# Kernel optimization log

Hardware: AMD Instinct MI355X
Metric: run time of the kernel (lower is better)

The kernel has to match this reference:

```python
import jax, jax.numpy as jnp
import numpy as np

T = 1024          # tokens (batch*seq, vLLM flattened layout)
D = 2048          # hidden_size
H = 16            # attention heads
HD = D // H       # head_dim = 128
E = 16            # num routed experts
K = 2             # top_k
IM = 1408         # moe_intermediate_size
IS = 5632         # shared_expert_intermediate_size
EPS = 1e-6
THETA = 10000.0


def setup_inputs() -> dict:
    key = jax.random.key(0)
    ks = jax.random.split(key, 14)
    s = 0.02  # weight scale
    n = jax.random.normal
    return {
        "positions": jnp.arange(T, dtype=jnp.int32),
        "hidden_states": n(ks[0], (T, D), jnp.float32),
        "ln1_w": 1.0 + s * n(ks[1], (D,), jnp.float32),
        "ln2_w": 1.0 + s * n(ks[2], (D,), jnp.float32),
        "qkv_w": s * n(ks[3], (D, 3 * H * HD), jnp.float32),
        "qkv_b": s * n(ks[4], (3 * H * HD,), jnp.float32),
        "o_w": s * n(ks[5], (H * HD, D), jnp.float32),
        "router_w": s * n(ks[6], (D, E), jnp.float32),
        "w_gate": s * n(ks[7], (E, D, IM), jnp.float32),
        "w_up": s * n(ks[8], (E, D, IM), jnp.float32),
        "w_down": s * n(ks[9], (E, IM, D), jnp.float32),
        "sh_gate_up": s * n(ks[10], (D, 2 * IS), jnp.float32),
        "sh_down": s * n(ks[11], (IS, D), jnp.float32),
        "sh_expert_gate": s * n(ks[12], (D, 1), jnp.float32),
    }


def _rmsnorm(x, w):
    var = jnp.mean(x * x, axis=-1, keepdims=True)
    return x * jax.lax.rsqrt(var + EPS) * w


def _rope(x, positions):
    # neox-style rotary: x [T, H, HD]
    half = HD // 2
    inv_freq = 1.0 / (THETA ** (jnp.arange(0, half, dtype=jnp.float32) / half * 1.0))
    inv_freq = 1.0 / (THETA ** (jnp.arange(0, HD, 2, dtype=jnp.float32) / HD))
    ang = positions.astype(jnp.float32)[:, None] * inv_freq  # [T, HD/2]
    cos = jnp.cos(ang)[:, None, :]
    sin = jnp.sin(ang)[:, None, :]
    x1, x2 = x[..., :half], x[..., half:]
    return jnp.concatenate([x1 * cos - x2 * sin, x2 * cos + x1 * sin], axis=-1)


def reference(positions, hidden_states, ln1_w, ln2_w, qkv_w, qkv_b, o_w,
              router_w, w_gate, w_up, w_down, sh_gate_up, sh_down,
              sh_expert_gate):
    # --- input RMSNorm (residual=None path) ---
    residual = hidden_states
    x = _rmsnorm(hidden_states, ln1_w)

    # --- self-attention: QKV + RoPE + causal SDPA + o_proj ---
    qkv = x @ qkv_w + qkv_b
    q, k, v = jnp.split(qkv, [H * HD, 2 * H * HD], axis=-1)
    q = _rope(q.reshape(T, H, HD), positions)
    k = _rope(k.reshape(T, H, HD), positions)
    v = v.reshape(T, H, HD)
    scale = HD ** -0.5
    scores = jnp.einsum('thd,shd->hts', q, k) * scale  # [H, T, T]
    causal = jnp.tril(jnp.ones((T, T), dtype=bool))
    scores = jnp.where(causal[None], scores, jnp.finfo(scores.dtype).min)
    attn = jax.nn.softmax(scores, axis=-1)
    ctx = jnp.einsum('hts,shd->thd', attn, v).reshape(T, H * HD)
    attn_out = ctx @ o_w

    # --- fused add + post-attention RMSNorm ---
    residual = residual + attn_out
    x = _rmsnorm(residual, ln2_w)

    # --- sparse MoE: router -> softmax -> top-k (renormalized) -> experts ---
    logits = x @ router_w                                    # [T, E]
    probs = jax.nn.softmax(logits.astype(jnp.float32), axis=-1)
    topv, topi = jax.lax.top_k(probs, K)                     # [T, K]
    topv = topv / jnp.sum(topv, axis=-1, keepdims=True)      # norm_topk_prob
    w = jnp.zeros((T, E), dtype=x.dtype).at[
        jnp.arange(T)[:, None], topi].set(topv.astype(x.dtype))
    g = jax.nn.silu(jnp.einsum('td,edi->tei', x, w_gate)) * \
        jnp.einsum('td,edi->tei', x, w_up)                   # [T, E, IM]
    moe_out = jnp.einsum('tei,eid,te->td', g, w_down, w)

    # --- shared expert with sigmoid gate ---
    gu = x @ sh_gate_up
    g2, u2 = jnp.split(gu, 2, axis=-1)
    shared = (jax.nn.silu(g2) * u2) @ sh_down
    shared = jax.nn.sigmoid(x @ sh_expert_gate) * shared

    hidden_states = moe_out + shared
    return hidden_states, residual
```

## Files before the change

### kernel.cpp

```cpp
#include <hip/hip_runtime.h>

constexpr int T_  = 1024;
constexpr int D_  = 2048;
constexpr int H_  = 16;
constexpr int HD_ = 128;
constexpr int E_  = 16;
constexpr int IM_ = 1408;
constexpr int IS_ = 5632;

typedef __attribute__((ext_vector_type(8))) short bf16x8;
typedef __attribute__((ext_vector_type(4))) short short4v;
typedef __attribute__((ext_vector_type(4))) float f32x4;

__device__ __forceinline__ short f2bf(float f){
  unsigned u = __builtin_bit_cast(unsigned, f);
  u += 0x7fffu + ((u >> 16) & 1u);
  return (short)(u >> 16);
}
__device__ __forceinline__ float bf2f(short s){
  unsigned u = ((unsigned)(unsigned short)s) << 16;
  return __builtin_bit_cast(float, u);
}
__device__ __forceinline__ f32x4 mfma16(bf16x8 a, bf16x8 b, f32x4 c){
  return __builtin_amdgcn_mfma_f32_16x16x32_bf16(a, b, c, 0, 0, 0);
}
__device__ __forceinline__ void split3(float f, short& h, short& m, short& l){
  h = f2bf(f); float r = f - bf2f(h);
  m = f2bf(r); l = f2bf(r - bf2f(m));
}
__device__ __forceinline__ void split2(float f, short& h, short& m){
  h = f2bf(f); m = f2bf(f - bf2f(h));
}

__global__ __launch_bounds__(256) void sctab_kernel(
    const int* __restrict__ pos, float* __restrict__ cst, float* __restrict__ snt)
{
  int idx = blockIdx.x * 256 + threadIdx.x;
  if (idx >= T_ * 64) return;
  int t = idx >> 6, i = idx & 63;
  float invf = (float)pow(10000.0, -(double)i / 64.0);
  float ang  = (float)pos[t] * invf;
  double s, c;
  sincos((double)ang, &s, &c);
  cst[idx] = (float)c; snt[idx] = (float)s;
}

__global__ __launch_bounds__(256) void rms_kernel(
    const float* __restrict__ x, const float* __restrict__ w,
    short* __restrict__ o0, short* __restrict__ o1, short* __restrict__ o2,
    short* __restrict__ ob, float* __restrict__ of)
{
  int t = blockIdx.x, tid = threadIdx.x;
  const float* xr = x + (size_t)t * D_;
  float4 va = ((const float4*)xr)[tid*2];
  float4 vb = ((const float4*)xr)[tid*2+1];
  float ss = va.x*va.x + va.y*va.y + va.z*va.z + va.w*va.w
           + vb.x*vb.x + vb.y*vb.y + vb.z*vb.z + vb.w*vb.w;
  for (int o = 32; o; o >>= 1) ss += __shfl_xor(ss, o, 64);
  __shared__ float red[4];
  int lane = tid & 63, wid = tid >> 6;
  if (lane == 0) red[wid] = ss;
  __syncthreads();
  ss = red[0] + red[1] + red[2] + red[3];
  float rs = 1.0f / sqrtf(ss * (1.0f/D_) + 1e-6f);
  float4 wa = ((const float4*)w)[tid*2];
  float4 wb = ((const float4*)w)[tid*2+1];
  float xv[8] = {va.x,va.y,va.z,va.w, vb.x,vb.y,vb.z,vb.w};
  float wv[8] = {wa.x,wa.y,wa.z,wa.w, wb.x,wb.y,wb.z,wb.w};
  size_t base = (size_t)t * D_ + tid*8;
  for (int j = 0; j < 8; ++j){
    float o = xv[j] * rs * wv[j];
    if (o0){
      short hh, mm, ll; split3(o, hh, mm, ll);
      o0[base+j] = hh; o1[base+j] = mm; o2[base+j] = ll;
    }
    if (ob) ob[base+j] = f2bf(o);
    if (of) of[base+j] = o;
  }
}

__global__ __launch_bounds__(256) void prepk_kernel(
    const float* __restrict__ qkv, const float* __restrict__ cst,
    const float* __restrict__ snt, short* __restrict__ Kp0, short* __restrict__ Kp1)
{
  int idx = blockIdx.x * 256 + threadIdx.x;
  int c = idx & 7, t = (idx >> 3) & (T_-1), h = idx >> 13;
  int d0 = c * 8;
  const float* kp = qkv + (size_t)t * (3*D_) + D_ + h*HD_;
  const float* cp = cst + t*64 + d0;
  const float* sp = snt + t*64 + d0;
  bf16x8 lh, ll, hh, hl;
  #pragma unroll
  for (int j = 0; j < 8; ++j){
    float xl = kp[d0+j], xh = kp[d0+64+j];
    float cv = cp[j], sv = sp[j];
    float rl = xl*cv - xh*sv, rh = xh*cv + xl*sv;
    short a, b;
    split2(rl, a, b); lh[j] = a; ll[j] = b;
    split2(rh, a, b); hh[j] = a; hl[j] = b;
  }
  size_t ob = ((size_t)h*T_ + t) * HD_;
  *(bf16x8*)(Kp0 + ob + d0)      = lh;
  *(bf16x8*)(Kp0 + ob + 64 + d0) = hh;
  *(bf16x8*)(Kp1 + ob + d0)      = ll;
  *(bf16x8*)(Kp1 + ob + 64 + d0) = hl;
}

__global__ __launch_bounds__(256) void prepv_kernel(
    const float* __restrict__ qkv, short* __restrict__ Vp0, short* __restrict__ Vp1)
{
  __shared__ short Vl[2][128][72];
  int t0 = blockIdx.x * 64, h = blockIdx.y, tid = threadIdx.x;
  int r = tid >> 2, cq = (tid & 3) * 32;
  const float* src = qkv + (size_t)(t0+r) * (3*D_) + 2*D_ + h*HD_ + cq;
  #pragma unroll
  for (int jj = 0; jj < 8; ++jj){
    float4 v = *(const float4*)(src + jj*4);
    float vv[4] = {v.x, v.y, v.z, v.w};
    #pragma unroll
    for (int u = 0; u < 4; ++u){
      int d = cq + jj*4 + u;
      short a, b; split2(vv[u], a, b);
      Vl[0][d][r] = a; Vl[1][d][r] = b;
    }
  }
  __syncthreads();
  int d = tid >> 1, tc = (tid & 1) * 32;
  short* dst0 = Vp0 + ((size_t)h*HD_ + d) * T_ + t0 + tc;
  short* dst1 = Vp1 + ((size_t)h*HD_ + d) * T_ + t0 + tc;
  #pragma unroll
  for (int q = 0; q < 4; ++q){
    *(uint4*)(dst0 + q*8) = *(const uint4*)&Vl[0][d][tc + q*8];
    *(uint4*)(dst1 + q*8) = *(const uint4*)&Vl[1][d][tc + q*8];
  }
}

__global__ __launch_bounds__(128) void attn_kernel(
    const float* __restrict__ qkv,
    const float* __restrict__ cst, const float* __restrict__ snt,
    const short* __restrict__ Kp0, const short* __restrict__ Kp1,
    const short* __restrict__ Vp0, const short* __restrict__ Vp1,
    short* __restrict__ c0p, short* __restrict__ c1p, short* __restrict__ c2p)
{
  __shared__ __attribute__((aligned(16))) short Ks[2][2][32][128];
  __shared__ __attribute__((aligned(16))) short Vs[2][2][128][40];
  __shared__ __attribute__((aligned(16))) short Ps[3][2][16][40];

  const float SCALE = 0.08838834764831845f;
  const int QW = 3*D_;
  int h = blockIdx.x;
  int ys = blockIdx.y;
  int qt = (ys < 16) ? (ys*2) : ((31-ys)*2 + 1);
  int q0 = qt * 32;
  int tid = threadIdx.x, lane = tid & 63, wq = tid >> 6;
  int lr = lane & 15, kq8 = (lane >> 4) * 8, r4 = (lane >> 4) * 4;

  bf16x8 qfh[4], qfm[4], qfl[4];
  { int qrow = q0 + wq*16 + lr;
    const float* qp = qkv + (size_t)qrow * QW + h*HD_;
    const float* cp = cst + qrow*64;
    const float* sp = snt + qrow*64;
    float x[4][8], cs[2][8], sn[2][8], rot[4][8];
    for (int ks = 0; ks < 4; ++ks)
      for (int j = 0; j < 8; ++j) x[ks][j] = qp[ks*32 + kq8 + j];
    for (int hf = 0; hf < 2; ++hf)
      for (int j = 0; j < 8; ++j){
        cs[hf][j] = cp[hf*32 + kq8 + j];
        sn[hf][j] = sp[hf*32 + kq8 + j];
      }
    for (int j = 0; j < 8; ++j){
      rot[0][j] = x[0][j]*cs[0][j] - x[2][j]*sn[0][j];
      rot[1][j] = x[1][j]*cs[1][j] - x[3][j]*sn[1][j];
      rot[2][j] = x[2][j]*cs[0][j] + x[0][j]*sn[0][j];
      rot[3][j] = x[3][j]*cs[1][j] + x[1][j]*sn[1][j];
    }
    for (int ks = 0; ks < 4; ++ks)
      for (int j = 0; j < 8; ++j){
        short a, b, c; split3(rot[ks][j], a, b, c);
        qfh[ks][j] = a; qfm[ks][j] = b; qfl[ks][j] = c;
      }
  }

  f32x4 acc[8];
  for (int i = 0; i < 8; ++i) acc[i] = f32x4{0.f,0.f,0.f,0.f};
  float mrun[4] = {-1e30f,-1e30f,-1e30f,-1e30f};
  float lrun[4] = {0.f,0.f,0.f,0.f};

  int krow = tid >> 2, kc = (tid & 3) * 32;
  const short* kb0 = Kp0 + ((size_t)h*T_ + krow) * HD_ + kc;
  const short* kb1 = Kp1 + ((size_t)h*T_ + krow) * HD_ + kc;
  const short* vb0 = Vp0 + ((size_t)h*HD_ + tid) * T_;
  const short* vb1 = Vp1 + ((size_t)h*HD_ + tid) * T_;
  int xr = (krow & 7) * 8;

  uint4 kr0[4], kr1[4], vr0[4], vr1[4];
  auto LOAD = [&](int it){
    size_t ko = (size_t)it * 32 * HD_;
    const uint4* p0 = (const uint4*)(kb0 + ko);
    const uint4* p1 = (const uint4*)(kb1 + ko);
    #pragma unroll
    for (int g = 0; g < 4; ++g){ kr0[g] = p0[g]; kr1[g] = p1[g]; }
    const uint4* q0p = (const uint4*)(vb0 + it*32);
    const uint4* q1p = (const uint4*)(vb1 + it*32);
    #pragma unroll
    for (int g = 0; g < 4; ++g){ vr0[g] = q0p[g]; vr1[g] = q1p[g]; }
  };
  auto STORE = [&](int buf){
    #pragma unroll
    for (int g = 0; g < 4; ++g){
      int col = (kc + 8*g) ^ xr;
      *(uint4*)&Ks[buf][0][krow][col] = kr0[g];
      *(uint4*)&Ks[buf][1][krow][col] = kr1[g];
    }
    #pragma unroll
    for (int g = 0; g < 4; ++g){
      *(uint4*)&Vs[buf][0][tid][g*8] = vr0[g];
      *(uint4*)&Vs[buf][1][tid][g*8] = vr1[g];
    }
  };

  int nt = qt + 1;
  LOAD(0); STORE(0);
  if (nt > 1) LOAD(1);
  asm volatile("s_waitcnt lgkmcnt(0)" ::: "memory");
  __builtin_amdgcn_s_barrier();

  int cur = 0;
  for (int it = 0; it < nt; ++it){
    if (it + 1 < nt){
      STORE(cur ^ 1);
      if (it + 2 < nt) LOAD(it + 2);
    }
    int kv0 = it * 32;
    int xl = (lr & 7) * 8;
    f32x4 s0 = f32x4{0.f,0.f,0.f,0.f}, s1 = f32x4{0.f,0.f,0.f,0.f};
    #pragma unroll
    for (int ks = 0; ks < 4; ++ks){
      int col = (ks*32 + kq8) ^ xl;
      bf16x8 b0h = *(const bf16x8*)&Ks[cur][0][lr][col];
      bf16x8 b0m = *(const bf16x8*)&Ks[cur][1][lr][col];
      bf16x8 b1h = *(const bf16x8*)&Ks[cur][0][16+lr][col];
      bf16x8 b1m = *(const bf16x8*)&Ks[cur][1][16+lr][col];
      s0 = mfma16(qfh[ks], b0h, s0); s0 = mfma16(qfh[ks], b0m, s0);
      s0 = mfma16(qfm[ks], b0h, s0); s0 = mfma16(qfm[ks], b0m, s0);
      s0 = mfma16(qfl[ks], b0h, s0);
      s1 = mfma16(qfh[ks], b1h, s1); s1 = mfma16(qfh[ks], b1m, s1);
      s1 = mfma16(qfm[ks], b1h, s1); s1 = mfma16(qfm[ks], b1m, s1);
      s1 = mfma16(qfl[ks], b1h, s1);
    }
    float pm[2][4]; float alpha[4];
    for (int r = 0; r < 4; ++r){
      int qr = q0 + wq*16 + r4 + r;
      float x0 = s0[r]*SCALE, x1 = s1[r]*SCALE;
      if (kv0 + lr > qr)      x0 = -1e30f;
      if (kv0 + 16 + lr > qr) x1 = -1e30f;
      float mt_ = fmaxf(x0, x1);
      mt_ = fmaxf(mt_, __shfl_xor(mt_, 1, 64));
      mt_ = fmaxf(mt_, __shfl_xor(mt_, 2, 64));
      mt_ = fmaxf(mt_, __shfl_xor(mt_, 4, 64));
      mt_ = fmaxf(mt_, __shfl_xor(mt_, 8, 64));
      float mn = fmaxf(mrun[r], mt_);
      float p0 = __expf(x0 - mn), p1 = __expf(x1 - mn);
      pm[0][r] = p0; pm[1][r] = p1;
      float ls = p0 + p1;
      ls += __shfl_xor(ls, 1, 64); ls += __shfl_xor(ls, 2, 64);
      ls += __shfl_xor(ls, 4, 64); ls += __shfl_xor(ls, 8, 64);
      alpha[r] = __expf(mrun[r] - mn);
      lrun[r] = lrun[r]*alpha[r] + ls;
      mrun[r] = mn;
    }
    for (int dt = 0; dt < 8; ++dt){
      f32x4 a = acc[dt];
      a[0]*=alpha[0]; a[1]*=alpha[1]; a[2]*=alpha[2]; a[3]*=alpha[3];
      acc[dt] = a;
    }
    for (int nn = 0; nn < 2; ++nn)
      for (int r = 0; r < 4; ++r){
        short a, b, c; split3(pm[nn][r], a, b, c);
        Ps[0][wq][r4+r][nn*16+lr] = a;
        Ps[1][wq][r4+r][nn*16+lr] = b;
        Ps[2][wq][r4+r][nn*16+lr] = c;
      }
    bf16x8 pah = *(const bf16x8*)&Ps[0][wq][lr][kq8];
    bf16x8 pam = *(const bf16x8*)&Ps[1][wq][lr][kq8];
    bf16x8 pal = *(const bf16x8*)&Ps[2][wq][lr][kq8];
    #pragma unroll
    for (int dt = 0; dt < 8; ++dt){
      bf16x8 vbh = *(const bf16x8*)&Vs[cur][0][dt*16+lr][kq8];
      bf16x8 vbm = *(const bf16x8*)&Vs[cur][1][dt*16+lr][kq8];
      acc[dt] = mfma16(pah, vbh, acc[dt]);
      acc[dt] = mfma16(pah, vbm, acc[dt]);
      acc[dt] = mfma16(pam, vbh, acc[dt]);
      acc[dt] = mfma16(pam, vbm, acc[dt]);
      acc[dt] = mfma16(pal, vbh, acc[dt]);
    }
    asm volatile("s_waitcnt lgkmcnt(0)" ::: "memory");
    __builtin_amdgcn_s_barrier();
    cur ^= 1;
  }
  for (int dt = 0; dt < 8; ++dt)
    for (int r = 0; r < 4; ++r){
      int qr = q0 + wq*16 + r4 + r;
      float o = acc[dt][r] / lrun[r];
      size_t ix = (size_t)qr * D_ + h*HD_ + dt*16 + lr;
      short a, b, c; split3(o, a, b, c);
      c0p[ix] = a; c1p[ix] = b; c2p[ix] = c;
    }
}

enum { M_QKV = 0, M_OPROJ = 1, M_GU_MOE = 2, M_GU_SH = 3, M_DN_MOE = 4, M_DN_SH = 5 };

template<int MODE>
__global__ __launch_bounds__(256) void gemm3_kernel(
    const short* __restrict__ A0, const short* __restrict__ A1, const short* __restrict__ A2,
    const float* __restrict__ Bw, const float* __restrict__ bias,
    const float* __restrict__ addsrc, float* __restrict__ outF,
    int K, int lda, int ldb, int ldo)
{
  __shared__ __attribute__((aligned(16))) short As[2][3][64][40];
  __shared__ __attribute__((aligned(16))) short Bs[2][2][64][40];

  int m0 = blockIdx.y * 64, n0 = blockIdx.x * 64;
  int tid = threadIdx.x, lane = tid & 63, wid = tid >> 6;
  int wm = wid >> 1, wn = wid & 1;
  int lr = lane & 15, kq8 = (lane >> 4) * 8;

  f32x4 acc[2][2];
  for (int i = 0; i < 2; ++i)
    for (int j = 0; j < 2; ++j) acc[i][j] = f32x4{0.f,0.f,0.f,0.f};

  int arow = tid >> 2, ac = (tid & 3) * 8;
  const short* aP0 = A0 + (size_t)(m0 + arow) * lda + ac;
  const short* aP1 = A1 + (size_t)(m0 + arow) * lda + ac;
  const short* aP2 = A2 + (size_t)(m0 + arow) * lda + ac;
  int bn = tid & 63, bk0 = (tid >> 6) * 8;
  const float* bP = Bw + n0 + bn;

  uint4 ar0, ar1, ar2; float br[8];
  auto LOAD = [&](int kt){
    ar0 = *(const uint4*)(aP0 + kt*32);
    ar1 = *(const uint4*)(aP1 + kt*32);
    ar2 = *(const uint4*)(aP2 + kt*32);
    const float* p = bP + (size_t)(kt*32 + bk0) * ldb;
    #pragma unroll
    for (int j = 0; j < 8; ++j) br[j] = p[(size_t)j * ldb];
  };
  auto STORE = [&](int buf){
    *(uint4*)&As[buf][0][arow][ac] = ar0;
    *(uint4*)&As[buf][1][arow][ac] = ar1;
    *(uint4*)&As[buf][2][arow][ac] = ar2;
    short hs[8], ms[8];
    #pragma unroll
    for (int j = 0; j < 8; ++j) split2(br[j], hs[j], ms[j]);
    *(short4v*)&Bs[buf][0][bn][bk0]   = short4v{hs[0],hs[1],hs[2],hs[3]};
    *(short4v*)&Bs[buf][0][bn][bk0+4] = short4v{hs[4],hs[5],hs[6],hs[7]};
    *(short4v*)&Bs[buf][1][bn][bk0]   = short4v{ms[0],ms[1],ms[2],ms[3]};
    *(short4v*)&Bs[buf][1][bn][bk0+4] = short4v{ms[4],ms[5],ms[6],ms[7]};
  };

  int NK = K / 32;
  LOAD(0); STORE(0);
  if (NK > 1) LOAD(1);
  asm volatile("s_waitcnt lgkmcnt(0)" ::: "memory");
  __builtin_amdgcn_s_barrier();

  int cur = 0;
  for (int kt = 0; kt < NK; ++kt){
    if (kt + 1 < NK){
      STORE(cur ^ 1);
      if (kt + 2 < NK) LOAD(kt + 2);
    }
    bf16x8 aH[2], aM[2], aL[2];
    #pragma unroll
    for (int mt = 0; mt < 2; ++mt){
      aH[mt] = *(const bf16x8*)&As[cur][0][wm*32 + mt*16 + lr][kq8];
      aM[mt] = *(const bf16x8*)&As[cur][1][wm*32 + mt*16 + lr][kq8];
      aL[mt] = *(const bf16x8*)&As[cur][2][wm*32 + mt*16 + lr][kq8];
    }
    #pragma unroll
    for (int nt = 0; nt < 2; ++nt){
      bf16x8 bH = *(const bf16x8*)&Bs[cur][0][wn*32 + nt*16 + lr][kq8];
      bf16x8 bM = *(const bf16x8*)&Bs[cur][1][wn*32 + nt*16 + lr][kq8];
      #pragma unroll
      for (int mt = 0; mt < 2; ++mt){
        f32x4 a = acc[mt][nt];
        a = mfma16(aH[mt], bH, a);
        a = mfma16(aH[mt], bM, a);
        a = mfma16(aM[mt], bH, a);
        a = mfma16(aM[mt], bM, a);
        a = mfma16(aL[mt], bH, a);
        acc[mt][nt] = a;
      }
    }
    asm volatile("s_waitcnt lgkmcnt(0)" ::: "memory");
    __builtin_amdgcn_s_barrier();
    cur ^= 1;
  }

  for (int mt = 0; mt < 2; ++mt)
    for (int nt = 0; nt < 2; ++nt)
      for (int r = 0; r < 4; ++r){
        int mrow = m0 + wm*32 + mt*16 + (lane >> 4)*4 + r;
        int col  = n0 + wn*32 + nt*16 + lr;
        float v = acc[mt][nt][r];
        if constexpr (MODE == M_QKV){
          outF[(size_t)mrow * ldo + col] = v + bias[col];
        } else {
          outF[(size_t)mrow * ldo + col] = v + addsrc[(size_t)mrow * ldo + col];
        }
      }
}

template<int MODE>
__global__ __launch_bounds__(256) void gemm2_kernel(
    const short* __restrict__ A0,
    const float* __restrict__ B0, const float* __restrict__ B1,
    float* __restrict__ outF, short* __restrict__ outB,
    const int* __restrict__ perm, const int* __restrict__ offE,
    const int* __restrict__ cntE, const float* __restrict__ wgt,
    const float* __restrict__ sig,
    int M, int K, int lda, int ldb, int ldo)
{
  constexpr bool DUAL = (MODE == M_GU_MOE || MODE == M_GU_SH);
  constexpr bool MOE  = (MODE == M_GU_MOE || MODE == M_DN_MOE);
  constexpr int NB = DUAL ? 2 : 1;
  constexpr int BN = 64, NT = 2;

  __shared__ __attribute__((aligned(16))) short As[2][128][40];
  __shared__ __attribute__((aligned(16))) short Bs[2][NB][BN][40];

  int e = blockIdx.z;
  int mcnt = M, mbase = 0;
  if constexpr (MOE){ mcnt = cntE[e]; mbase = offE[e]; }
  int m0 = blockIdx.y * 128;
  if (m0 >= mcnt) return;
  int n0 = blockIdx.x * BN;

  const float* Bq0 = B0;
  const float* Bq1 = B1;
  if constexpr (MOE){
    Bq0 += (size_t)e * K * ldb;
    if constexpr (DUAL) Bq1 += (size_t)e * K * ldb;
  }

  int tid = threadIdx.x, lane = tid & 63, wid = tid >> 6;
  int wm = wid >> 1, wn = wid & 1;
  int lr = lane & 15, kq8 = (lane >> 4) * 8;

  f32x4 acc0[4][NT], acc1[4][NT];
  #pragma unroll
  for (int i = 0; i < 4; ++i)
    #pragma unroll
    for (int j = 0; j < NT; ++j){
      acc0[i][j] = f32x4{0.f,0.f,0.f,0.f};
      if constexpr (DUAL) acc1[i][j] = f32x4{0.f,0.f,0.f,0.f};
    }

  int arow = tid >> 1, acol = (tid & 1) * 16;
  int aRowIdx;
  { int mr = m0 + arow;
    if constexpr (MODE == M_GU_MOE)      aRowIdx = perm[mbase + ((mr < mcnt) ? mr : 0)];
    else if constexpr (MODE == M_DN_MOE) aRowIdx = mbase + ((mr < mcnt) ? mr : 0);
    else                                 aRowIdx = mr;
  }
  const short* aP = A0 + (size_t)aRowIdx * lda;

  int bn_ = tid & 63, bkq = (tid >> 6) * 8;
  const float* bP0 = Bq0 + n0 + bn_;
  const float* bP1 = DUAL ? (Bq1 + n0 + bn_) : nullptr;

  uint4 arA, arB;
  float br0[8], br1[8];

  auto LOAD = [&](int kt){
    const uint4* s = (const uint4*)(aP + kt*32 + acol);
    arA = s[0]; arB = s[1];
    const float* p0 = bP0 + (size_t)(kt*32 + bkq) * ldb;
    #pragma unroll
    for (int j = 0; j < 8; ++j) br0[j] = p0[(size_t)j * ldb];
    if constexpr (DUAL){
      const float* p1 = bP1 + (size_t)(kt*32 + bkq) * ldb;
      #pragma unroll
      for (int j = 0; j < 8; ++j) br1[j] = p1[(size_t)j * ldb];
    }
  };
  auto STORE = [&](int buf){
    *(uint4*)&As[buf][arow][acol]   = arA;
    *(uint4*)&As[buf][arow][acol+8] = arB;
    bf16x8 v0;
    #pragma unroll
    for (int j = 0; j < 8; ++j) v0[j] = f2bf(br0[j]);
    *(bf16x8*)&Bs[buf][0][bn_][bkq] = v0;
    if constexpr (DUAL){
      bf16x8 v1;
      #pragma unroll
      for (int j = 0; j < 8; ++j) v1[j] = f2bf(br1[j]);
      *(bf16x8*)&Bs[buf][1][bn_][bkq] = v1;
    }
  };

  int NK = K / 32;
  LOAD(0);
  STORE(0);
  if (NK > 1) LOAD(1);
  asm volatile("s_waitcnt lgkmcnt(0)" ::: "memory");
  __builtin_amdgcn_s_barrier();

  int cur = 0;
  for (int kt = 0; kt < NK; ++kt){
    if (kt + 1 < NK){
      STORE(cur ^ 1);
      if (kt + 2 < NK) LOAD(kt + 2);
    }
    bf16x8 a[4];
    #pragma unroll
    for (int mt = 0; mt < 4; ++mt)
      a[mt] = *(const bf16x8*)&As[cur][wm*64 + mt*16 + lr][kq8];
    #pragma unroll
    for (int nt = 0; nt < NT; ++nt){
      int nrow = wn*32 + nt*16 + lr;
      bf16x8 b0 = *(const bf16x8*)&Bs[cur][0][nrow][kq8];
      #pragma unroll
      for (int mt = 0; mt < 4; ++mt)
        acc0[mt][nt] = mfma16(a[mt], b0, acc0[mt][nt]);
      if constexpr (DUAL){
        bf16x8 b1 = *(const bf16x8*)&Bs[cur][1][nrow][kq8];
        #pragma unroll
        for (int mt = 0; mt < 4; ++mt)
          acc1[mt][nt] = mfma16(a[mt], b1, acc1[mt][nt]);
      }
    }
    asm volatile("s_waitcnt lgkmcnt(0)" ::: "memory");
    __builtin_amdgcn_s_barrier();
    cur ^= 1;
  }

  for (int mt = 0; mt < 4; ++mt)
    #pragma unroll
    for (int nt = 0; nt < NT; ++nt)
      for (int r = 0; r < 4; ++r){
        int mrow = m0 + wm*64 + mt*16 + (lane >> 4)*4 + r;
        if (mrow >= mcnt) continue;
        int col = n0 + wn*32 + nt*16 + lr;
        float v = acc0[mt][nt][r];
        if constexpr (DUAL){
          float u = acc1[mt][nt][r];
          float sv = v / (1.f + __expf(-v)) * u;
          outB[(size_t)(mbase + mrow) * ldo + col] = f2bf(sv);
        } else if constexpr (MODE == M_DN_MOE){
          int tk = perm[mbase + mrow];
          atomicAdd(&outF[(size_t)tk * ldo + col], v * wgt[mbase + mrow]);
        } else {
          size_t ix = (size_t)mrow * ldo + col;
          outF[ix] = outF[ix] + sig[mrow] * v;
        }
      }
}

__global__ __launch_bounds__(256) void router_kernel(
    const float* __restrict__ x2f, const float* __restrict__ rw,
    const float* __restrict__ seg, int* __restrict__ te, float* __restrict__ tw,
    float* __restrict__ sig, int* __restrict__ cnt)
{
  int t = blockIdx.x, tid = threadIdx.x, lane = tid & 63, w = tid >> 6;
  const float* xr = x2f + (size_t)t * D_;
  float a0 = 0.f, a1 = 0.f, a2 = 0.f, a3 = 0.f, ag = 0.f;
  for (int j = 0; j < 32; ++j){
    int d = lane + 64*j;
    float xv = xr[d];
    const float* rp = rw + (size_t)d * E_ + w*4;
    a0 += xv * rp[0]; a1 += xv * rp[1]; a2 += xv * rp[2]; a3 += xv * rp[3];
    ag += xv * seg[d];
  }
  for (int o = 32; o; o >>= 1){
    a0 += __shfl_xor(a0, o, 64); a1 += __shfl_xor(a1, o, 64);
    a2 += __shfl_xor(a2, o, 64); a3 += __shfl_xor(a3, o, 64);
    ag += __shfl_xor(ag, o, 64);
  }
  __shared__ float lg[16];
  __shared__ float sgv;
  if (lane == 0){
    lg[w*4+0] = a0; lg[w*4+1] = a1; lg[w*4+2] = a2; lg[w*4+3] = a3;
    if (w == 0) sgv = ag;
  }
  __syncthreads();
  if (tid == 0){
    int e0 = 0; float v0 = lg[0];
    for (int ee = 1; ee < 16; ++ee) if (lg[ee] > v0){ v0 = lg[ee]; e0 = ee; }
    int e1 = -1; float v1 = -3e38f;
    for (int ee = 0; ee < 16; ++ee){
      if (ee == e0) continue;
      if (lg[ee] > v1){ v1 = lg[ee]; e1 = ee; }
    }
    float w0 = 1.f / (1.f + expf(v1 - v0));
    te[2*t] = e0; te[2*t+1] = e1;
    tw[2*t] = w0; tw[2*t+1] = 1.f - w0;
    atomicAdd(&cnt[e0], 1); atomicAdd(&cnt[e1], 1);
    sig[t] = 1.f / (1.f + expf(-sgv));
  }
}

__global__ void prefix_kernel(const int* __restrict__ cnt, int* __restrict__ offE,
                              int* __restrict__ cursor)
{
  if (threadIdx.x == 0){
    int s = 0;
    for (int e = 0; e < 16; ++e){ offE[e] = s; s += cnt[e]; }
  }
  if (threadIdx.x < 16) cursor[threadIdx.x] = 0;
}

__global__ __launch_bounds__(256) void scatter_kernel(
    const int* __restrict__ te, const float* __restrict__ tw,
    const int* __restrict__ offE, int* __restrict__ cursor,
    int* __restrict__ perm, float* __restrict__ wgt)
{
  int t = blockIdx.x * 256 + threadIdx.x;
  if (t >= T_) return;
  for (int i = 0; i < 2; ++i){
    int e = te[2*t + i];
    int pos = offE[e] + atomicAdd(&cursor[e], 1);
    perm[pos] = t; wgt[pos] = tw[2*t + i];
  }
}

extern "C" void kernel_launch(void* const* d_in, const int* in_sizes, int n_in,
                              void* d_out, int out_size, void* d_ws, size_t ws_size,
                              hipStream_t stream)
{
  const int*   positions = (const int*)  d_in[0];
  const float* hidden    = (const float*)d_in[1];
  const float* ln1       = (const float*)d_in[2];
  const float* ln2       = (const float*)d_in[3];
  const float* qkv_w     = (const float*)d_in[4];
  const float* qkv_b     = (const float*)d_in[5];
  const float* o_w       = (const float*)d_in[6];
  const float* router_w  = (const float*)d_in[7];
  const float* w_gate    = (const float*)d_in[8];
  const float* w_up      = (const float*)d_in[9];
  const float* w_down    = (const float*)d_in[10];
  const float* sh_gu     = (const float*)d_in[11];
  const float* sh_down   = (const float*)d_in[12];
  const float* sh_eg     = (const float*)d_in[13];

  float* out_hidden = (float*)d_out;
  float* out_resid  = (float*)d_out + (size_t)T_ * D_;

  char* wp = (char*)d_ws;
  auto alloc = [&](size_t b){ char* p = wp; wp += (b + 255) & ~(size_t)255; return p; };

  float* qkv  = (float*)alloc((size_t)T_ * 3*D_ * 4);
  short* x1h  = (short*)alloc((size_t)T_ * D_ * 2);
  short* x1m  = (short*)alloc((size_t)T_ * D_ * 2);
  short* x1l  = (short*)alloc((size_t)T_ * D_ * 2);
  short* Kp0  = (short*)alloc((size_t)T_ * D_ * 2);
  short* Kp1  = (short*)alloc((size_t)T_ * D_ * 2);
  short* Vp0  = (short*)alloc((size_t)T_ * D_ * 2);
  short* Vp1  = (short*)alloc((size_t)T_ * D_ * 2);
  float* cst  = (float*)alloc((size_t)T_ * 64 * 4);
  float* snt  = (float*)alloc((size_t)T_ * 64 * 4);
  int*   te   = (int*)  alloc(2*T_*4);
  float* tw   = (float*)alloc(2*T_*4);
  float* sig  = (float*)alloc(T_*4);
  int*   cnt    = (int*)alloc(256);
  int*   offE   = (int*)alloc(256);
  int*   cursor = (int*)alloc(256);
  int*   perm = (int*)  alloc(2*T_*4);
  float* wgt  = (float*)alloc(2*T_*4);

  short* ctxh = x1h;
  short* ctxm = x1m;
  short* ctxl = x1l;
  float* x2f  = qkv;
  short* sbuf = (short*)((char*)qkv + (size_t)8388608);
  short* gbuf = (short*)x1h;
  short* x2b  = (short*)((char*)x1h + (size_t)5767168);

  hipMemsetAsync(cnt, 0, 64, stream);
  hipMemsetAsync(out_hidden, 0, (size_t)T_ * D_ * 4, stream);

  sctab_kernel<<<(T_*64)/256, 256, 0, stream>>>(positions, cst, snt);

  rms_kernel<<<T_, 256, 0, stream>>>(hidden, ln1, x1h, x1m, x1l, nullptr, nullptr);

  gemm3_kernel<M_QKV><<<dim3(96, 16), 256, 0, stream>>>(
      x1h, x1m, x1l, qkv_w, qkv_b, nullptr, qkv, D_, D_, 3*D_, 3*D_);

  prepk_kernel<<<(T_*H_*8)/256, 256, 0, stream>>>(qkv, cst, snt, Kp0, Kp1);
  prepv_kernel<<<dim3(16, 16), 256, 0, stream>>>(qkv, Vp0, Vp1);

  attn_kernel<<<dim3(16, 32), 128, 0, stream>>>(
      qkv, cst, snt, Kp0, Kp1, Vp0, Vp1, ctxh, ctxm, ctxl);

  gemm3_kernel<M_OPROJ><<<dim3(32, 16), 256, 0, stream>>>(
      ctxh, ctxm, ctxl, o_w, nullptr, hidden, out_resid, D_, D_, D_, D_);

  rms_kernel<<<T_, 256, 0, stream>>>(out_resid, ln2, nullptr, nullptr, nullptr, x2b, x2f);

  router_kernel<<<T_, 256, 0, stream>>>(x2f, router_w, sh_eg, te, tw, sig, cnt);
  prefix_kernel<<<1, 64, 0, stream>>>(cnt, offE, cursor);
  scatter_kernel<<<4, 256, 0, stream>>>(te, tw, offE, cursor, perm, wgt);

  gemm2_kernel<M_GU_MOE><<<dim3(22, 8, 16), 256, 0, stream>>>(
      x2b, w_gate, w_up, nullptr, gbuf,
      perm, offE, cnt, nullptr, nullptr, T_, D_, D_, IM_, IM_);

  gemm2_kernel<M_DN_MOE><<<dim3(32, 8, 16), 256, 0, stream>>>(
      gbuf, w_down, nullptr, out_hidden, nullptr,
      perm, offE, cnt, wgt, nullptr, T_, IM_, IM_, D_, D_);

  gemm2_kernel<M_GU_SH><<<dim3(88, 8, 1), 256, 0, stream>>>(
      x2b, sh_gu, sh_gu + IS_, nullptr, sbuf,
      nullptr, nullptr, nullptr, nullptr, nullptr, T_, D_, D_, 2*IS_, IS_);

  gemm2_kernel<M_DN_SH><<<dim3(32, 8, 1), 256, 0, stream>>>(
      sbuf, sh_down, nullptr, out_hidden, nullptr,
      nullptr, nullptr, nullptr, nullptr, sig, T_, IS_, IS_, D_, D_);

  (void)in_sizes; (void)n_in; (void)out_size; (void)ws_size;
}
```

Baseline: 903.0 us.

## Merge MoE and shared-expert GEMMs, prepack o_proj weights, use packed bf16 converts

Result: faster. 876.3 us (-3.0%).

```diff
diff --git a/kernel.cpp b/kernel.cpp
--- a/kernel.cpp
+++ b/kernel.cpp
@@ -21,6 +21,17 @@
   unsigned u = ((unsigned)(unsigned short)s) << 16;
   return __builtin_bit_cast(float, u);
 }
+__device__ __forceinline__ unsigned cvtpk(float lo, float hi){
+  unsigned r;
+  asm("v_cvt_pk_bf16_f32 %0, %1, %2" : "=v"(r) : "v"(lo), "v"(hi));
+  return r;
+}
+__device__ __forceinline__ float pk_lo(unsigned h){
+  return __builtin_bit_cast(float, h << 16);
+}
+__device__ __forceinline__ float pk_hi(unsigned h){
+  return __builtin_bit_cast(float, h & 0xffff0000u);
+}
 __device__ __forceinline__ f32x4 mfma16(bf16x8 a, bf16x8 b, f32x4 c){
   return __builtin_amdgcn_mfma_f32_16x16x32_bf16(a, b, c, 0, 0, 0);
 }
@@ -30,6 +41,9 @@
 }
 __device__ __forceinline__ void split2(float f, short& h, short& m){
   h = f2bf(f); m = f2bf(f - bf2f(h));
+}
+__device__ __forceinline__ uint4 mk4(unsigned a, unsigned b, unsigned c, unsigned d){
+  uint4 r; r.x=a; r.y=b; r.z=c; r.w=d; return r;
 }
 
 __global__ __launch_bounds__(256) void sctab_kernel(
@@ -68,14 +82,21 @@
   float xv[8] = {va.x,va.y,va.z,va.w, vb.x,vb.y,vb.z,vb.w};
   float wv[8] = {wa.x,wa.y,wa.z,wa.w, wb.x,wb.y,wb.z,wb.w};
   size_t base = (size_t)t * D_ + tid*8;
-  for (int j = 0; j < 8; ++j){
-    float o = xv[j] * rs * wv[j];
+  #pragma unroll
+  for (int p = 0; p < 4; ++p){
+    float f0 = xv[2*p]   * rs * wv[2*p];
+    float f1 = xv[2*p+1] * rs * wv[2*p+1];
     if (o0){
-      short hh, mm, ll; split3(o, hh, mm, ll);
-      o0[base+j] = hh; o1[base+j] = mm; o2[base+j] = ll;
-    }
-    if (ob) ob[base+j] = f2bf(o);
-    if (of) of[base+j] = o;
+      unsigned h = cvtpk(f0, f1);
+      float r0 = f0 - pk_lo(h), r1 = f1 - pk_hi(h);
+      unsigned m = cvtpk(r0, r1);
+      unsigned l = cvtpk(r0 - pk_lo(m), r1 - pk_hi(m));
+      *(unsigned*)&o0[base + 2*p] = h;
+      *(unsigned*)&o1[base + 2*p] = m;
+      *(unsigned*)&o2[base + 2*p] = l;
+    }
+    if (ob) *(unsigned*)&ob[base + 2*p] = cvtpk(f0, f1);
+    if (of){ of[base + 2*p] = f0; of[base + 2*p + 1] = f1; }
   }
 }
 
@@ -89,21 +110,24 @@
   const float* kp = qkv + (size_t)t * (3*D_) + D_ + h*HD_;
   const float* cp = cst + t*64 + d0;
   const float* sp = snt + t*64 + d0;
-  bf16x8 lh, ll, hh, hl;
+  unsigned lh[4], ll[4], hh[4], hl[4];
   #pragma unroll
-  for (int j = 0; j < 8; ++j){
-    float xl = kp[d0+j], xh = kp[d0+64+j];
-    float cv = cp[j], sv = sp[j];
-    float rl = xl*cv - xh*sv, rh = xh*cv + xl*sv;
-    short a, b;
-    split2(rl, a, b); lh[j] = a; ll[j] = b;
-    split2(rh, a, b); hh[j] = a; hl[j] = b;
+  for (int p = 0; p < 4; ++p){
+    float xl0 = kp[d0+2*p],    xh0 = kp[d0+64+2*p];
+    float xl1 = kp[d0+2*p+1],  xh1 = kp[d0+64+2*p+1];
+    float cv0 = cp[2*p], sv0 = sp[2*p], cv1 = cp[2*p+1], sv1 = sp[2*p+1];
+    float rl0 = xl0*cv0 - xh0*sv0, rh0 = xh0*cv0 + xl0*sv0;
+    float rl1 = xl1*cv1 - xh1*sv1, rh1 = xh1*cv1 + xl1*sv1;
+    unsigned a = cvtpk(rl0, rl1);
+    ll[p] = cvtpk(rl0 - pk_lo(a), rl1 - pk_hi(a)); lh[p] = a;
+    unsigned b = cvtpk(rh0, rh1);
+    hl[p] = cvtpk(rh0 - pk_lo(b), rh1 - pk_hi(b)); hh[p] = b;
   }
   size_t ob = ((size_t)h*T_ + t) * HD_;
-  *(bf16x8*)(Kp0 + ob + d0)      = lh;
-  *(bf16x8*)(Kp0 + ob + 64 + d0) = hh;
-  *(bf16x8*)(Kp1 + ob + d0)      = ll;
-  *(bf16x8*)(Kp1 + ob + 64 + d0) = hl;
+  *(uint4*)(Kp0 + ob + d0)      = mk4(lh[0],lh[1],lh[2],lh[3]);
+  *(uint4*)(Kp0 + ob + 64 + d0) = mk4(hh[0],hh[1],hh[2],hh[3]);
+  *(uint4*)(Kp1 + ob + d0)      = mk4(ll[0],ll[1],ll[2],ll[3]);
+  *(uint4*)(Kp1 + ob + 64 + d0) = mk4(hl[0],hl[1],hl[2],hl[3]);
 }
 
 __global__ __launch_bounds__(256) void prepv_kernel(
@@ -133,6 +157,35 @@
     *(uint4*)(dst0 + q*8) = *(const uint4*)&Vl[0][d][tc + q*8];
     *(uint4*)(dst1 + q*8) = *(const uint4*)&Vl[1][d][tc + q*8];
   }
+}
+
+__global__ __launch_bounds__(256) void prepw_kernel(
+    const float* __restrict__ w, short* __restrict__ P0, short* __restrict__ P1)
+{
+  __shared__ short L0[64][72], L1[64][72];
+  int k0 = blockIdx.x * 64, n0 = blockIdx.y * 64;
+  int tid = threadIdx.x;
+  int r = tid >> 2, cq = (tid & 3) * 16;
+  const float* src = w + (size_t)(k0 + r) * D_ + n0 + cq;
+  #pragma unroll
+  for (int q = 0; q < 4; ++q){
+    float4 f = *(const float4*)(src + q*4);
+    float fv[4] = {f.x, f.y, f.z, f.w};
+    #pragma unroll
+    for (int u = 0; u < 4; ++u){
+      int n = cq + q*4 + u;
+      short a, b; split2(fv[u], a, b);
+      L0[n][r] = a; L1[n][r] = b;
+    }
+  }
+  __syncthreads();
+  int n = tid >> 2, kq = (tid & 3) * 16;
+  short* d0 = P0 + (size_t)(n0 + n) * D_ + k0 + kq;
+  short* d1 = P1 + (size_t)(n0 + n) * D_ + k0 + kq;
+  *(uint4*)(d0)     = *(const uint4*)&L0[n][kq];
+  *(uint4*)(d0 + 8) = *(const uint4*)&L0[n][kq + 8];
+  *(uint4*)(d1)     = *(const uint4*)&L1[n][kq];
+  *(uint4*)(d1 + 8) = *(const uint4*)&L1[n][kq + 8];
 }
 
 __global__ __launch_bounds__(128) void attn_kernel(
@@ -308,13 +361,15 @@
     }
 }
 
-enum { M_QKV = 0, M_OPROJ = 1, M_GU_MOE = 2, M_GU_SH = 3, M_DN_MOE = 4, M_DN_SH = 5 };
+enum { M_QKV = 0, M_OPROJ = 1 };
 
 template<int MODE>
 __global__ __launch_bounds__(256) void gemm3_kernel(
     const short* __restrict__ A0, const short* __restrict__ A1, const short* __restrict__ A2,
-    const float* __restrict__ Bw, const float* __restrict__ bias,
-    const float* __restrict__ addsrc, float* __restrict__ outF,
+    const float* __restrict__ Bw,
+    const short* __restrict__ Bp0, const short* __restrict__ Bp1,
+    const float* __restrict__ bias, const float* __restrict__ addsrc,
+    float* __restrict__ outF,
     int K, int lda, int ldb, int ldo)
 {
   __shared__ __attribute__((aligned(16))) short As[2][3][64][40];
@@ -334,28 +389,46 @@
   const short* aP1 = A1 + (size_t)(m0 + arow) * lda + ac;
   const short* aP2 = A2 + (size_t)(m0 + arow) * lda + ac;
   int bn = tid & 63, bk0 = (tid >> 6) * 8;
-  const float* bP = Bw + n0 + bn;
-
-  uint4 ar0, ar1, ar2; float br[8];
+  const float* bP  = Bw  ? (Bw + n0 + bn) : nullptr;
+  const short* bq0 = Bp0 ? (Bp0 + (size_t)(n0 + bn) * K) : nullptr;
+  const short* bq1 = Bp1 ? (Bp1 + (size_t)(n0 + bn) * K) : nullptr;
+
+  uint4 ar0, ar1, ar2;
+  float br[8];
+  uint4 pb0, pb1;
+
   auto LOAD = [&](int kt){
     ar0 = *(const uint4*)(aP0 + kt*32);
     ar1 = *(const uint4*)(aP1 + kt*32);
     ar2 = *(const uint4*)(aP2 + kt*32);
-    const float* p = bP + (size_t)(kt*32 + bk0) * ldb;
-    #pragma unroll
-    for (int j = 0; j < 8; ++j) br[j] = p[(size_t)j * ldb];
+    if constexpr (MODE == M_QKV){
+      const float* p = bP + (size_t)(kt*32 + bk0) * ldb;
+      #pragma unroll
+      for (int j = 0; j < 8; ++j) br[j] = p[(size_t)j * ldb];
+    } else {
+      pb0 = *(const uint4*)(bq0 + kt*32 + bk0);
+      pb1 = *(const uint4*)(bq1 + kt*32 + bk0);
+    }
   };
   auto STORE = [&](int buf){
     *(uint4*)&As[buf][0][arow][ac] = ar0;
     *(uint4*)&As[buf][1][arow][ac] = ar1;
     *(uint4*)&As[buf][2][arow][ac] = ar2;
-    short hs[8], ms[8];
-    #pragma unroll
-    for (int j = 0; j < 8; ++j) split2(br[j], hs[j], ms[j]);
-    *(short4v*)&Bs[buf][0][bn][bk0]   = short4v{hs[0],hs[1],hs[2],hs[3]};
-    *(short4v*)&Bs[buf][0][bn][bk0+4] = short4v{hs[4],hs[5],hs[6],hs[7]};
-    *(short4v*)&Bs[buf][1][bn][bk0]   = short4v{ms[0],ms[1],ms[2],ms[3]};
-    *(short4v*)&Bs[buf][1][bn][bk0+4] = short4v{ms[4],ms[5],ms[6],ms[7]};
+    if constexpr (MODE == M_QKV){
+      unsigned hh[4], mm[4];
+      #pragma unroll
+      for (int p = 0; p < 4; ++p){
+        float f0 = br[2*p], f1 = br[2*p+1];
+        unsigned h = cvtpk(f0, f1);
+        mm[p] = cvtpk(f0 - pk_lo(h), f1 - pk_hi(h));
+        hh[p] = h;
+      }
+      *(uint4*)&Bs[buf][0][bn][bk0] = mk4(hh[0],hh[1],hh[2],hh[3]);
+      *(uint4*)&Bs[buf][1][bn][bk0] = mk4(mm[0],mm[1],mm[2],mm[3]);
+    } else {
+      *(uint4*)&Bs[buf][0][bn][bk0] = pb0;
+      *(uint4*)&Bs[buf][1][bn][bk0] = pb1;
+    }
   };
 
   int NK = K / 32;
@@ -411,63 +484,55 @@
       }
 }
 
-template<int MODE>
-__global__ __launch_bounds__(256) void gemm2_kernel(
-    const short* __restrict__ A0,
-    const float* __restrict__ B0, const float* __restrict__ B1,
-    float* __restrict__ outF, short* __restrict__ outB,
+__global__ __launch_bounds__(256) void gu_kernel(
+    const short* __restrict__ x2b,
+    const float* __restrict__ w_gate, const float* __restrict__ w_up,
+    const float* __restrict__ sh_gu,
+    short* __restrict__ gbuf, short* __restrict__ sbuf,
     const int* __restrict__ perm, const int* __restrict__ offE,
-    const int* __restrict__ cntE, const float* __restrict__ wgt,
-    const float* __restrict__ sig,
-    int M, int K, int lda, int ldb, int ldo)
-{
-  constexpr bool DUAL = (MODE == M_GU_MOE || MODE == M_GU_SH);
-  constexpr bool MOE  = (MODE == M_GU_MOE || MODE == M_DN_MOE);
-  constexpr int NB = DUAL ? 2 : 1;
-  constexpr int BN = 64, NT = 2;
-
+    const int* __restrict__ cntE)
+{
   __shared__ __attribute__((aligned(16))) short As[2][128][40];
-  __shared__ __attribute__((aligned(16))) short Bs[2][NB][BN][40];
-
-  int e = blockIdx.z;
-  int mcnt = M, mbase = 0;
-  if constexpr (MOE){ mcnt = cntE[e]; mbase = offE[e]; }
+  __shared__ __attribute__((aligned(16))) short Bs[2][2][64][40];
+
+  int z = blockIdx.z;
+  bool SH = (z == E_);
+  int N    = SH ? IS_ : IM_;
+  int n0 = blockIdx.x * 64;
+  if (n0 >= N) return;
+  int mcnt  = SH ? T_ : cntE[z];
+  int mbase = SH ? 0  : offE[z];
   int m0 = blockIdx.y * 128;
   if (m0 >= mcnt) return;
-  int n0 = blockIdx.x * BN;
-
-  const float* Bq0 = B0;
-  const float* Bq1 = B1;
-  if constexpr (MOE){
-    Bq0 += (size_t)e * K * ldb;
-    if constexpr (DUAL) Bq1 += (size_t)e * K * ldb;
-  }
+  int ldb = SH ? 2*IS_ : IM_;
+  int ldo = SH ? IS_   : IM_;
+  const float* Bg = SH ? sh_gu        : (w_gate + (size_t)z * D_ * IM_);
+  const float* Bu = SH ? (sh_gu + IS_) : (w_up  + (size_t)z * D_ * IM_);
+  short* outB = SH ? sbuf : gbuf;
 
   int tid = threadIdx.x, lane = tid & 63, wid = tid >> 6;
   int wm = wid >> 1, wn = wid & 1;
   int lr = lane & 15, kq8 = (lane >> 4) * 8;
 
-  f32x4 acc0[4][NT], acc1[4][NT];
+  f32x4 acc0[4][2], acc1[4][2];
   #pragma unroll
   for (int i = 0; i < 4; ++i)
-    #pragma unroll
-    for (int j = 0; j < NT; ++j){
+    for (int j = 0; j < 2; ++j){
       acc0[i][j] = f32x4{0.f,0.f,0.f,0.f};
-      if constexpr (DUAL) acc1[i][j] = f32x4{0.f,0.f,0.f,0.f};
+      acc1[i][j] = f32x4{0.f,0.f,0.f,0.f};
     }
 
   int arow = tid >> 1, acol = (tid & 1) * 16;
   int aRowIdx;
   { int mr = m0 + arow;
-    if constexpr (MODE == M_GU_MOE)      aRowIdx = perm[mbase + ((mr < mcnt) ? mr : 0)];
-    else if constexpr (MODE == M_DN_MOE) aRowIdx = mbase + ((mr < mcnt) ? mr : 0);
-    else                                 aRowIdx = mr;
-  }
-  const short* aP = A0 + (size_t)aRowIdx * lda;
+    int mc = (mr < mcnt) ? mr : 0;
+    aRowIdx = SH ? mc : perm[mbase + mc];
+  }
+  const short* aP = x2b + (size_t)aRowIdx * D_;
 
   int bn_ = tid & 63, bkq = (tid >> 6) * 8;
-  const float* bP0 = Bq0 + n0 + bn_;
-  const float* bP1 = DUAL ? (Bq1 + n0 + bn_) : nullptr;
+  const float* bP0 = Bg + n0 + bn_;
+  const float* bP1 = Bu + n0 + bn_;
 
   uint4 arA, arB;
   float br0[8], br1[8];
@@ -476,33 +541,26 @@
     const uint4* s = (const uint4*)(aP + kt*32 + acol);
     arA = s[0]; arB = s[1];
     const float* p0 = bP0 + (size_t)(kt*32 + bkq) * ldb;
-    #pragma unroll
-    for (int j = 0; j < 8; ++j) br0[j] = p0[(size_t)j * ldb];
-    if constexpr (DUAL){
-      const float* p1 = bP1 + (size_t)(kt*32 + bkq) * ldb;
-      #pragma unroll
-      for (int j = 0; j < 8; ++j) br1[j] = p1[(size_t)j * ldb];
-    }
+    const float* p1 = bP1 + (size_t)(kt*32 + bkq) * ldb;
+    #pragma unroll
+    for (int j = 0; j < 8; ++j){ br0[j] = p0[(size_t)j * ldb]; br1[j] = p1[(size_t)j * ldb]; }
   };
   auto STORE = [&](int buf){
     *(uint4*)&As[buf][arow][acol]   = arA;
     *(uint4*)&As[buf][arow][acol+8] = arB;
-    bf16x8 v0;
-    #pragma unroll
-    for (int j = 0; j < 8; ++j) v0[j] = f2bf(br0[j]);
-    *(bf16x8*)&Bs[buf][0][bn_][bkq] = v0;
-    if constexpr (DUAL){
-      bf16x8 v1;
-      #pragma unroll
-      for (int j = 0; j < 8; ++j) v1[j] = f2bf(br1[j]);
-      *(bf16x8*)&Bs[buf][1][bn_][bkq] = v1;
-    }
+    unsigned v0[4], v1[4];
+    #pragma unroll
+    for (int p = 0; p < 4; ++p){
+      v0[p] = cvtpk(br0[2*p], br0[2*p+1]);
+      v1[p] = cvtpk(br1[2*p], br1[2*p+1]);
+    }
+    *(uint4*)&Bs[buf][0][bn_][bkq] = mk4(v0[0],v0[1],v0[2],v0[3]);
+    *(uint4*)&Bs[buf][1][bn_][bkq] = mk4(v1[0],v1[1],v1[2],v1[3]);
   };
 
-  int NK = K / 32;
-  LOAD(0);
-  STORE(0);
-  if (NK > 1) LOAD(1);
+  constexpr int NK = D_ / 32;
+  LOAD(0); STORE(0);
+  LOAD(1);
   asm volatile("s_waitcnt lgkmcnt(0)" ::: "memory");
   __builtin_amdgcn_s_barrier();
 
@@ -517,17 +575,14 @@
     for (int mt = 0; mt < 4; ++mt)
       a[mt] = *(const bf16x8*)&As[cur][wm*64 + mt*16 + lr][kq8];
     #pragma unroll
-    for (int nt = 0; nt < NT; ++nt){
+    for (int nt = 0; nt < 2; ++nt){
       int nrow = wn*32 + nt*16 + lr;
       bf16x8 b0 = *(const bf16x8*)&Bs[cur][0][nrow][kq8];
+      bf16x8 b1 = *(const bf16x8*)&Bs[cur][1][nrow][kq8];
       #pragma unroll
-      for (int mt = 0; mt < 4; ++mt)
+      for (int mt = 0; mt < 4; ++mt){
         acc0[mt][nt] = mfma16(a[mt], b0, acc0[mt][nt]);
-      if constexpr (DUAL){
-        bf16x8 b1 = *(const bf16x8*)&Bs[cur][1][nrow][kq8];
-        #pragma unroll
-        for (int mt = 0; mt < 4; ++mt)
-          acc1[mt][nt] = mfma16(a[mt], b1, acc1[mt][nt]);
+        acc1[mt][nt] = mfma16(a[mt], b1, acc1[mt][nt]);
       }
     }
     asm volatile("s_waitcnt lgkmcnt(0)" ::: "memory");
@@ -536,23 +591,116 @@
   }
 
   for (int mt = 0; mt < 4; ++mt)
-    #pragma unroll
-    for (int nt = 0; nt < NT; ++nt)
+    for (int nt = 0; nt < 2; ++nt)
       for (int r = 0; r < 4; ++r){
         int mrow = m0 + wm*64 + mt*16 + (lane >> 4)*4 + r;
         if (mrow >= mcnt) continue;
         int col = n0 + wn*32 + nt*16 + lr;
         float v = acc0[mt][nt][r];
-        if constexpr (DUAL){
-          float u = acc1[mt][nt][r];
-          float sv = v / (1.f + __expf(-v)) * u;
-          outB[(size_t)(mbase + mrow) * ldo + col] = f2bf(sv);
-        } else if constexpr (MODE == M_DN_MOE){
+        float u = acc1[mt][nt][r];
+        float sv = v / (1.f + __expf(-v)) * u;
+        outB[(size_t)(mbase + mrow) * ldo + col] = f2bf(sv);
+      }
+}
+
+__global__ __launch_bounds__(256) void dn_kernel(
+    const short* __restrict__ gbuf, const short* __restrict__ sbuf,
+    const float* __restrict__ w_down, const float* __restrict__ sh_down,
+    float* __restrict__ outF,
+    const int* __restrict__ perm, const int* __restrict__ offE,
+    const int* __restrict__ cntE, const float* __restrict__ wgt,
+    const float* __restrict__ sig)
+{
+  __shared__ __attribute__((aligned(16))) short As[2][128][40];
+  __shared__ __attribute__((aligned(16))) short Bs[2][64][40];
+
+  int z = blockIdx.z;
+  bool SH = (z == E_);
+  int K = SH ? IS_ : IM_;
+  int mcnt  = SH ? T_ : cntE[z];
+  int mbase = SH ? 0  : offE[z];
+  int m0 = blockIdx.y * 128;
+  if (m0 >= mcnt) return;
+  int n0 = blockIdx.x * 64;
+  const float* Bq = SH ? sh_down : (w_down + (size_t)z * IM_ * D_);
+  const short* Ab = SH ? sbuf : gbuf;
+
+  int tid = threadIdx.x, lane = tid & 63, wid = tid >> 6;
+  int wm = wid >> 1, wn = wid & 1;
+  int lr = lane & 15, kq8 = (lane >> 4) * 8;
+
+  f32x4 acc0[4][2];
+  #pragma unroll
+  for (int i = 0; i < 4; ++i)
+    for (int j = 0; j < 2; ++j) acc0[i][j] = f32x4{0.f,0.f,0.f,0.f};
+
+  int arow = tid >> 1, acol = (tid & 1) * 16;
+  int mr = m0 + arow;
+  int mc = (mr < mcnt) ? mr : 0;
+  const short* aP = Ab + (size_t)(SH ? mc : (mbase + mc)) * K;
+
+  int bn_ = tid & 63, bkq = (tid >> 6) * 8;
+  const float* bP0 = Bq + n0 + bn_;
+
+  uint4 arA, arB;
+  float br0[8];
+
+  auto LOAD = [&](int kt){
+    const uint4* s = (const uint4*)(aP + kt*32 + acol);
+    arA = s[0]; arB = s[1];
+    const float* p0 = bP0 + (size_t)(kt*32 + bkq) * D_;
+    #pragma unroll
+    for (int j = 0; j < 8; ++j) br0[j] = p0[(size_t)j * D_];
+  };
+  auto STORE = [&](int buf){
+    *(uint4*)&As[buf][arow][acol]   = arA;
+    *(uint4*)&As[buf][arow][acol+8] = arB;
+    unsigned v0[4];
+    #pragma unroll
+    for (int p = 0; p < 4; ++p) v0[p] = cvtpk(br0[2*p], br0[2*p+1]);
+    *(uint4*)&Bs[buf][bn_][bkq] = mk4(v0[0],v0[1],v0[2],v0[3]);
+  };
+
+  int NK = K / 32;
+  LOAD(0); STORE(0);
+  LOAD(1);
+  asm volatile("s_waitcnt lgkmcnt(0)" ::: "memory");
+  __builtin_amdgcn_s_barrier();
+
+  int cur = 0;
+  for (int kt = 0; kt < NK; ++kt){
+    if (kt + 1 < NK){
+      STORE(cur ^ 1);
+      if (kt + 2 < NK) LOAD(kt + 2);
+    }
+    bf16x8 a[4];
+    #pragma unroll
+    for (int mt = 0; mt < 4; ++mt)
+      a[mt] = *(const bf16x8*)&As[cur][wm*64 + mt*16 + lr][kq8];
+    #pragma unroll
+    for (int nt = 0; nt < 2; ++nt){
+      bf16x8 b0 = *(const bf16x8*)&Bs[cur][wn*32 + nt*16 + lr][kq8];
+      #pragma unroll
+      for (int mt = 0; mt < 4; ++mt)
+        acc0[mt][nt] = mfma16(a[mt], b0, acc0[mt][nt]);
+    }
+    asm volatile("s_waitcnt lgkmcnt(0)" ::: "memory");
+    __builtin_amdgcn_s_barrier();
+    cur ^= 1;
+  }
+
+  for (int mt = 0; mt < 4; ++mt)
+    for (int nt = 0; nt < 2; ++nt)
+      for (int r = 0; r < 4; ++r){
+        int mrow = m0 + wm*64 + mt*16 + (lane >> 4)*4 + r;
+        if (mrow >= mcnt) continue;
+        int col = n0 + wn*32 + nt*16 + lr;
+        float v = acc0[mt][nt][r];
+        if (SH){
+          atomicAdd(&outF[(size_t)mrow * D_ + col], sig[mrow] * v);
+        } else {
           int tk = perm[mbase + mrow];
-          atomicAdd(&outF[(size_t)tk * ldo + col], v * wgt[mbase + mrow]);
-        } else {
-          size_t ix = (size_t)mrow * ldo + col;
-          outF[ix] = outF[ix] + sig[mrow] * v;
+          atomicAdd(&outF[(size_t)tk * D_ + col], v * wgt[mbase + mrow]);
         }
       }
 }
@@ -675,6 +823,8 @@
   short* sbuf = (short*)((char*)qkv + (size_t)8388608);
   short* gbuf = (short*)x1h;
   short* x2b  = (short*)((char*)x1h + (size_t)5767168);
+  short* Wo0  = Kp0;
+  short* Wo1  = Vp0;
 
   hipMemsetAsync(cnt, 0, 64, stream);
   hipMemsetAsync(out_hidden, 0, (size_t)T_ * D_ * 4, stream);
@@ -684,7 +834,8 @@
   rms_kernel<<<T_, 256, 0, stream>>>(hidden, ln1, x1h, x1m, x1l, nullptr, nullptr);
 
   gemm3_kernel<M_QKV><<<dim3(96, 16), 256, 0, stream>>>(
-      x1h, x1m, x1l, qkv_w, qkv_b, nullptr, qkv, D_, D_, 3*D_, 3*D_);
+      x1h, x1m, x1l, qkv_w, nullptr, nullptr, qkv_b, nullptr, qkv,
+      D_, D_, 3*D_, 3*D_);
 
   prepk_kernel<<<(T_*H_*8)/256, 256, 0, stream>>>(qkv, cst, snt, Kp0, Kp1);
   prepv_kernel<<<dim3(16, 16), 256, 0, stream>>>(qkv, Vp0, Vp1);
@@ -692,8 +843,11 @@
   attn_kernel<<<dim3(16, 32), 128, 0, stream>>>(
       qkv, cst, snt, Kp0, Kp1, Vp0, Vp1, ctxh, ctxm, ctxl);
 
+  prepw_kernel<<<dim3(32, 32), 256, 0, stream>>>(o_w, Wo0, Wo1);
+
   gemm3_kernel<M_OPROJ><<<dim3(32, 16), 256, 0, stream>>>(
-      ctxh, ctxm, ctxl, o_w, nullptr, hidden, out_resid, D_, D_, D_, D_);
+      ctxh, ctxm, ctxl, nullptr, Wo0, Wo1, nullptr, hidden, out_resid,
+      D_, D_, D_, D_);
 
   rms_kernel<<<T_, 256, 0, stream>>>(out_resid, ln2, nullptr, nullptr, nullptr, x2b, x2f);
 
@@ -701,21 +855,11 @@
   prefix_kernel<<<1, 64, 0, stream>>>(cnt, offE, cursor);
   scatter_kernel<<<4, 256, 0, stream>>>(te, tw, offE, cursor, perm, wgt);
 
-  gemm2_kernel<M_GU_MOE><<<dim3(22, 8, 16), 256, 0, stream>>>(
-      x2b, w_gate, w_up, nullptr, gbuf,
-      perm, offE, cnt, nullptr, nullptr, T_, D_, D_, IM_, IM_);
-
-  gemm2_kernel<M_DN_MOE><<<dim3(32, 8, 16), 256, 0, stream>>>(
-      gbuf, w_down, nullptr, out_hidden, nullptr,
-      perm, offE, cnt, wgt, nullptr, T_, IM_, IM_, D_, D_);
-
-  gemm2_kernel<M_GU_SH><<<dim3(88, 8, 1), 256, 0, stream>>>(
-      x2b, sh_gu, sh_gu + IS_, nullptr, sbuf,
-      nullptr, nullptr, nullptr, nullptr, nullptr, T_, D_, D_, 2*IS_, IS_);
-
-  gemm2_kernel<M_DN_SH><<<dim3(32, 8, 1), 256, 0, stream>>>(
-      sbuf, sh_down, nullptr, out_hidden, nullptr,
-      nullptr, nullptr, nullptr, nullptr, sig, T_, IS_, IS_, D_, D_);
+  gu_kernel<<<dim3(88, 8, 17), 256, 0, stream>>>(
+      x2b, w_gate, w_up, sh_gu, gbuf, sbuf, perm, offE, cnt);
+
+  dn_kernel<<<dim3(32, 8, 17), 256, 0, stream>>>(
+      gbuf, sbuf, w_down, sh_down, out_hidden, perm, offE, cnt, wgt, sig);
 
   (void)in_sizes; (void)n_in; (void)out_size; (void)ws_size;
 }
```
